# Kernel optimization log

Hardware: AMD Instinct MI355X
Metric: run time of the kernel (lower is better)

## Reference

```python
import jax, jax.numpy as jnp
import numpy as np

N = 50000      # nodes
E = 800000     # edges (avg degree 16)
IN = 64        # in_channels
OUT = 64       # out_channels
K = 3          # Chebyshev order
LAM = 2.0      # lambda_max for sym normalization


def setup_inputs() -> dict:
    key = jax.random.key(0)
    ks = jax.random.split(key, 16)
    s_in = 1.0 / np.sqrt(IN)
    s_out = 1.0 / np.sqrt(OUT)
    inp = {
        "X": jax.random.normal(ks[0], (N, IN), jnp.float32),
        "edge_index": jax.random.randint(ks[1], (2, E), 0, N, dtype=jnp.int64),
        "edge_weight": jax.random.uniform(ks[2], (E,), jnp.float32),
        # six ChebConv weight stacks [K, in, out] and biases [out]
        "W_xz": jax.random.normal(ks[3], (K, IN, OUT), jnp.float32) * s_in,
        "W_hz": jax.random.normal(ks[4], (K, OUT, OUT), jnp.float32) * s_out,
        "W_xr": jax.random.normal(ks[5], (K, IN, OUT), jnp.float32) * s_in,
        "W_hr": jax.random.normal(ks[6], (K, OUT, OUT), jnp.float32) * s_out,
        "W_xh": jax.random.normal(ks[7], (K, IN, OUT), jnp.float32) * s_in,
        "W_hh": jax.random.normal(ks[8], (K, OUT, OUT), jnp.float32) * s_out,
        "b_xz": jnp.zeros((OUT,), jnp.float32),
        "b_hz": jnp.zeros((OUT,), jnp.float32),
        "b_xr": jnp.zeros((OUT,), jnp.float32),
        "b_hr": jnp.zeros((OUT,), jnp.float32),
        "b_xh": jnp.zeros((OUT,), jnp.float32),
        "b_hh": jnp.zeros((OUT,), jnp.float32),
    }
    return inp


def _cheb_norm(edge_index, edge_weight):
    # PyG ChebConv __norm__ with sym normalization, lambda_max = 2:
    # L_hat = (2/lam) * (I - D^-1/2 A D^-1/2) - I
    src, dst = edge_index[0], edge_index[1]
    deg = jax.ops.segment_sum(edge_weight, src, num_segments=N)
    dinv = jnp.where(deg > 0, jax.lax.rsqrt(jnp.where(deg > 0, deg, 1.0)), 0.0)
    w_off = -(2.0 / LAM) * edge_weight * dinv[src] * dinv[dst]
    diag = 2.0 / LAM - 1.0  # 0 when lambda_max == 2
    return src, dst, w_off, diag


def _spmm(x, src, dst, w_off, diag):
    # y[i] = sum_{e: dst[e]=i} w_off[e] * x[src[e]] + diag * x[i]
    msg = w_off[:, None] * x[src]
    return jax.ops.segment_sum(msg, dst, num_segments=N) + diag * x


def _cheb_conv(x, W, b, src, dst, w_off, diag):
    Tx0 = x
    out = Tx0 @ W[0]
    Tx1 = _spmm(Tx0, src, dst, w_off, diag)
    out = out + Tx1 @ W[1]
    for k in range(2, K):
        Tx2 = 2.0 * _spmm(Tx1, src, dst, w_off, diag) - Tx0
        out = out + Tx2 @ W[k]
        Tx0, Tx1 = Tx1, Tx2
    return out + b


def reference(X, edge_index, edge_weight,
              W_xz, W_hz, W_xr, W_hr, W_xh, W_hh,
              b_xz, b_hz, b_xr, b_hr, b_xh, b_hh):
    src, dst, w_off, diag = _cheb_norm(edge_index, edge_weight)
    cheb = lambda x, W, b: _cheb_conv(x, W, b, src, dst, w_off, diag)
    H = jnp.zeros((N, OUT), X.dtype)  # _set_hidden_state with H=None
    Z = jax.nn.sigmoid(cheb(X, W_xz, b_xz) + cheb(H, W_hz, b_hz))
    R = jax.nn.sigmoid(cheb(X, W_xr, b_xr) + cheb(H, W_hr, b_hr))
    H_tilde = jnp.tanh(cheb(X, W_xh, b_xh) + cheb(H * R, W_hh, b_hh))
    H_new = Z * H + (1.0 - Z) * H_tilde
    return H_new
```

## Files before the change

### kernel.cpp

```cpp
#include <hip/hip_runtime.h>


#define N_NODES 50000
#define E_EDGES 800000
#define NC 64
#define BSH 6
#define BUKN 64
#define NBUK 782
#define EPB 2048
#define NBLK 391

#define OFF_CV       0
#define OFF_ROWSTART 1600000
#define OFF_TOTD     1650016
#define OFF_BASED    1650800
#define OFF_TOTS     1651584
#define OFF_BASES    1652368
#define OFF_TX1      1653152
#define OFF_RECD     1653152
#define OFF_DINV     3253152
#define OFF_CNTD     3303168
#define OFF_TX2      4853152
#define OFF_RECS     4853152
#define OFF_CNTS     6453152
#define OFF_WB       8053152

typedef __attribute__((ext_vector_type(8))) short bf16x8;
typedef __attribute__((ext_vector_type(4))) float f32x4;

__device__ __forceinline__ unsigned bf16rne(float x) {
    unsigned u = __float_as_uint(x);
    return (u + 0x7fffu + ((u >> 16) & 1u)) >> 16;
}

__global__ __launch_bounds__(256) void k_hist(const int* __restrict__ ei,
        int* __restrict__ cntD, int* __restrict__ cntS) {
    __shared__ int hD[NBUK], hS[NBUK];
    int t = threadIdx.x, blk = blockIdx.x;
    for (int b = t; b < NBUK; b += 256) { hD[b] = 0; hS[b] = 0; }
    __syncthreads();
    int e0 = blk * EPB;
    #pragma unroll
    for (int i = 0; i < 8; ++i) {
        int e = e0 + i * 256 + t;
        if (e < E_EDGES) {
            atomicAdd(&hS[ei[e] >> BSH], 1);
            atomicAdd(&hD[ei[E_EDGES + e] >> BSH], 1);
        }
    }
    __syncthreads();
    for (int b = t; b < NBUK; b += 256) {
        cntD[b * NBLK + blk] = hD[b];
        cntS[b * NBLK + blk] = hS[b];
    }
}

__global__ __launch_bounds__(256) void k_scanPB(int* __restrict__ cntD,
        int* __restrict__ cntS, int* __restrict__ totD, int* __restrict__ totS) {
    __shared__ int s[512];
    int t = threadIdx.x;
    int row = blockIdx.x; int* cnt; int* tot;
    if (row < NBUK) { cnt = cntD; tot = totD; }
    else            { row -= NBUK; cnt = cntS; tot = totS; }
    int v0 = (t < NBLK) ? cnt[row * NBLK + t] : 0;
    int v1 = (256 + t < NBLK) ? cnt[row * NBLK + 256 + t] : 0;
    s[t] = v0; s[256 + t] = v1;
    __syncthreads();
    for (int off = 1; off < 512; off <<= 1) {
        int a = (t >= off) ? s[t - off] : 0;
        int b = (256 + t >= off) ? s[256 + t - off] : 0;
        __syncthreads();
        s[t] += a; s[256 + t] += b;
        __syncthreads();
    }
    if (t < NBLK) cnt[row * NBLK + t] = s[t] - v0;
    if (256 + t < NBLK) cnt[row * NBLK + 256 + t] = s[256 + t] - v1;
    if (t == 0) tot[row] = s[511];
}

__global__ __launch_bounds__(256) void k_scanTot(int* __restrict__ totD,
        int* __restrict__ baseD, int* __restrict__ totS, int* __restrict__ baseS) {
    __shared__ int s[1024];
    int t = threadIdx.x;
    int* tot  = blockIdx.x ? totS  : totD;
    int* base = blockIdx.x ? baseS : baseD;
    int v[4];
    #pragma unroll
    for (int q = 0; q < 4; ++q) {
        int i = q * 256 + t;
        v[q] = (i < NBUK) ? tot[i] : 0;
        s[i] = v[q];
    }
    __syncthreads();
    for (int off = 1; off < 1024; off <<= 1) {
        int a[4];
        #pragma unroll
        for (int q = 0; q < 4; ++q) {
            int i = q * 256 + t;
            a[q] = (i >= off) ? s[i - off] : 0;
        }
        __syncthreads();
        #pragma unroll
        for (int q = 0; q < 4; ++q) s[q * 256 + t] += a[q];
        __syncthreads();
    }
    #pragma unroll
    for (int q = 0; q < 4; ++q) {
        int i = q * 256 + t;
        if (i < NBUK) base[i] = s[i] - v[q];
    }
}

__global__ __launch_bounds__(256) void k_scatter(const int* __restrict__ ei,
        const float* __restrict__ ew, const int* __restrict__ offD,
        const int* __restrict__ offS, const int* __restrict__ baseD,
        const int* __restrict__ baseS, long long* __restrict__ recD,
        long long* __restrict__ recS) {
    __shared__ int curD[NBUK], curS[NBUK];
    int t = threadIdx.x, blk = blockIdx.x;
    for (int b = t; b < NBUK; b += 256) {
        curD[b] = baseD[b] + offD[b * NBLK + blk];
        curS[b] = baseS[b] + offS[b * NBLK + blk];
    }
    __syncthreads();
    int e0 = blk * EPB;
    #pragma unroll
    for (int i = 0; i < 8; ++i) {
        int e = e0 + i * 256 + t;
        if (e < E_EDGES) {
            int sN = ei[e], dN = ei[E_EDGES + e];
            long long wb = (long long)(unsigned)__float_as_uint(ew[e]) << 32;
            int pD = atomicAdd(&curD[dN >> BSH], 1);
            recD[pD] = wb | (unsigned)((sN << BSH) | (dN & (BUKN - 1)));
            int pS = atomicAdd(&curS[sN >> BSH], 1);
            recS[pS] = wb | (unsigned)(sN & (BUKN - 1));
        }
    }
}

__global__ __launch_bounds__(256) void k_deg(const long long* __restrict__ recS,
        const int* __restrict__ totS, const int* __restrict__ baseS,
        float* __restrict__ dinv) {
    __shared__ float degL[BUKN];
    int t = threadIdx.x, b = blockIdx.x;
    if (t < BUKN) degL[t] = 0.f;
    __syncthreads();
    int st = baseS[b], n = totS[b];
    for (int i = t; i < n; i += 256) {
        long long r = recS[st + i];
        atomicAdd(&degL[(int)(r & (BUKN - 1))], __uint_as_float((unsigned)(r >> 32)));
    }
    __syncthreads();
    if (t < BUKN) {
        int node = b * BUKN + t;
        if (node < N_NODES) {
            float dg = degL[t];
            dinv[node] = dg > 0.f ? rsqrtf(dg) : 0.f;
        }
    }
}

__global__ __launch_bounds__(256) void k_csr(const long long* __restrict__ recD,
        const int* __restrict__ totD, const int* __restrict__ baseD,
        const float* __restrict__ dinv, long long* __restrict__ cv,
        int* __restrict__ row_start) {
    __shared__ int cnt[BUKN], rb[BUKN], cur[BUKN];
    __shared__ float dL[BUKN];
    int t = threadIdx.x, b = blockIdx.x;
    if (t < BUKN) {
        cnt[t] = 0;
        int node = b * BUKN + t;
        dL[t] = (node < N_NODES) ? dinv[node] : 0.f;
    }
    __syncthreads();
    int st = baseD[b], n = totD[b];
    for (int i = t; i < n; i += 256)
        atomicAdd(&cnt[(int)(recD[st + i] & (BUKN - 1))], 1);
    __syncthreads();
    if (t < BUKN) {
        int x = cnt[t];
        int orig = x;
        #pragma unroll
        for (int off = 1; off < BUKN; off <<= 1) {
            int v = __shfl_up(x, off, 64);
            if ((t & 63) >= off) x += v;
        }
        rb[t] = x - orig;
        cur[t] = x - orig;
        int node = b * BUKN + t;
        if (node < N_NODES) row_start[node] = st + (x - orig);
    }
    if (b == 0 && t == 0) row_start[N_NODES] = E_EDGES;
    __syncthreads();
    for (int i = t; i < n; i += 256) {
        long long r = recD[st + i];
        int m = (int)(r & 0xffffffffLL);
        float w = __uint_as_float((unsigned)(r >> 32));
        int rr = m & (BUKN - 1);
        int sN = m >> BSH;
        float val = -w * dinv[sN] * dL[rr];
        int pos = st + atomicAdd(&cur[rr], 1);
        cv[pos] = ((long long)__float_as_int(val) << 32) | (unsigned)sN;
    }
}

template<int SCALE, int SUB>
__global__ __launch_bounds__(256) void k_spmm(
        const int* __restrict__ row_start, const long long* __restrict__ cv,
        const float* __restrict__ xin, const float* __restrict__ xprev,
        float* __restrict__ out) {
    int wid = (blockIdx.x << 2) + (threadIdx.x >> 6);
    int lane = threadIdx.x & 63;
    if (wid >= N_NODES) return;
    int start = row_start[wid];
    int end   = row_start[wid + 1];
    float acc = 0.f;
    #pragma unroll 4
    for (int j = start; j < end; ++j) {
        long long p = cv[j];
        int s = (int)(p & 0xffffffffLL);
        float wv = __int_as_float((int)(p >> 32));
        acc = fmaf(wv, xin[(size_t)s * NC + lane], acc);
    }
    float r = (float)SCALE * acc;
    if (SUB) r -= xprev[(size_t)wid * NC + lane];
    out[(size_t)wid * NC + lane] = r;
}

__global__ __launch_bounds__(256) void k_prepw(const float* __restrict__ Wz,
        const float* __restrict__ Wh, short* __restrict__ WB) {
    int mg = blockIdx.x;
    int m = mg >> 1, g = mg & 1;
    const float* W = (g ? Wh : Wz) + m * 4096;
    int t = threadIdx.x;
    #pragma unroll
    for (int r = 0; r < 16; ++r) {
        int idx = r * 256 + t;
        int c = idx >> 6, o = idx & 63;
        float x = W[idx];
        unsigned hi = bf16rne(x);
        float fhi = __uint_as_float(hi << 16);
        unsigned lo = bf16rne(x - fhi);
        WB[(mg * 2 + 0) * 4096 + o * 64 + c] = (short)hi;
        WB[(mg * 2 + 1) * 4096 + o * 64 + c] = (short)lo;
    }
}

__global__ __launch_bounds__(256) void k_gru(
        const float* __restrict__ X, const float* __restrict__ Tx1,
        const float* __restrict__ Tx2, const short* __restrict__ WB,
        const float* __restrict__ bxz, const float* __restrict__ bhz,
        const float* __restrict__ bxh, const float* __restrict__ bhh,
        float* __restrict__ out) {
    __shared__ short Ahi[64 * 64];
    __shared__ short Alo[64 * 64];
    int tid = threadIdx.x;
    int l = tid & 63;
    int w = tid >> 6;
    int node0 = blockIdx.x * 64;

    f32x4 accz[4], acch[4];
    #pragma unroll
    for (int mt = 0; mt < 4; ++mt) {
        accz[mt] = (f32x4){0.f, 0.f, 0.f, 0.f};
        acch[mt] = (f32x4){0.f, 0.f, 0.f, 0.f};
    }

    const float* ins[3] = {X, Tx1, Tx2};
    #pragma unroll 1
    for (int m = 0; m < 3; ++m) {
        __syncthreads();
        const float* ip = ins[m];
        #pragma unroll
        for (int r = 0; r < 4; ++r) {
            int fidx = r * 256 + tid;
            int n = fidx >> 4, c4 = fidx & 15;
            int gn = node0 + n;
            float4 v = make_float4(0.f, 0.f, 0.f, 0.f);
            if (gn < N_NODES) v = *(const float4*)&ip[(size_t)gn * 64 + c4 * 4];
            unsigned h0 = bf16rne(v.x), h1 = bf16rne(v.y),
                     h2 = bf16rne(v.z), h3 = bf16rne(v.w);
            unsigned q0 = bf16rne(v.x - __uint_as_float(h0 << 16));
            unsigned q1 = bf16rne(v.y - __uint_as_float(h1 << 16));
            unsigned q2 = bf16rne(v.z - __uint_as_float(h2 << 16));
            unsigned q3 = bf16rne(v.w - __uint_as_float(h3 << 16));
            int kk = (c4 * 4) ^ ((n & 7) << 3);
            *(uint2*)&Ahi[n * 64 + kk] = make_uint2(h0 | (h1 << 16), h2 | (h3 << 16));
            *(uint2*)&Alo[n * 64 + kk] = make_uint2(q0 | (q1 << 16), q2 | (q3 << 16));
        }
        __syncthreads();
        const short* wbm = WB + m * 4 * 4096;
        #pragma unroll
        for (int kt = 0; kt < 2; ++kt) {
            int k0 = kt * 32 + (l >> 4) * 8;
            bf16x8 ah[4], al[4];
            #pragma unroll
            for (int mt = 0; mt < 4; ++mt) {
                int row = mt * 16 + (l & 15);
                int kk = k0 ^ ((row & 7) << 3);
                ah[mt] = *(const bf16x8*)&Ahi[row * 64 + kk];
                al[mt] = *(const bf16x8*)&Alo[row * 64 + kk];
            }
            int o = w * 16 + (l & 15);
            {
                bf16x8 bh_ = *(const bf16x8*)&wbm[0 * 4096 + o * 64 + k0];
                bf16x8 bl_ = *(const bf16x8*)&wbm[1 * 4096 + o * 64 + k0];
                #pragma unroll
                for (int mt = 0; mt < 4; ++mt) {
                    accz[mt] = __builtin_amdgcn_mfma_f32_16x16x32_bf16(ah[mt], bh_, accz[mt], 0, 0, 0);
                    accz[mt] = __builtin_amdgcn_mfma_f32_16x16x32_bf16(ah[mt], bl_, accz[mt], 0, 0, 0);
                    accz[mt] = __builtin_amdgcn_mfma_f32_16x16x32_bf16(al[mt], bh_, accz[mt], 0, 0, 0);
                }
            }
            {
                bf16x8 bh_ = *(const bf16x8*)&wbm[2 * 4096 + o * 64 + k0];
                bf16x8 bl_ = *(const bf16x8*)&wbm[3 * 4096 + o * 64 + k0];
                #pragma unroll
                for (int mt = 0; mt < 4; ++mt) {
                    acch[mt] = __builtin_amdgcn_mfma_f32_16x16x32_bf16(ah[mt], bh_, acch[mt], 0, 0, 0);
                    acch[mt] = __builtin_amdgcn_mfma_f32_16x16x32_bf16(ah[mt], bl_, acch[mt], 0, 0, 0);
                    acch[mt] = __builtin_amdgcn_mfma_f32_16x16x32_bf16(al[mt], bh_, acch[mt], 0, 0, 0);
                }
            }
        }
    }

    int o = w * 16 + (l & 15);
    float bz = bxz[o] + bhz[o];
    float bh = bxh[o] + bhh[o];
    #pragma unroll
    for (int mt = 0; mt < 4; ++mt) {
        #pragma unroll
        for (int r = 0; r < 4; ++r) {
            int node = node0 + mt * 16 + (l >> 4) * 4 + r;
            if (node < N_NODES) {
                float z = accz[mt][r] + bz;
                float h = acch[mt][r] + bh;
                float sig = 1.f / (1.f + __expf(-z));
                float e2 = __expf(-2.f * h);
                float th = (1.f - e2) / (1.f + e2);
                out[(size_t)node * 64 + o] = (1.f - sig) * th;
            }
        }
    }
}

extern "C" void kernel_launch(void* const* d_in, const int* in_sizes, int n_in,
                              void* d_out, int out_size, void* d_ws, size_t ws_size,
                              hipStream_t stream) {
    const float* X   = (const float*)d_in[0];
    const int*   ei  = (const int*)d_in[1];
    const float* ew  = (const float*)d_in[2];
    const float* Wxz = (const float*)d_in[3];
    const float* Wxh = (const float*)d_in[7];
    const float* bxz = (const float*)d_in[9];
    const float* bhz = (const float*)d_in[10];
    const float* bxh = (const float*)d_in[13];
    const float* bhh = (const float*)d_in[14];
    float* out = (float*)d_out;

    float* ws_f = (float*)d_ws;
    int*   ws_i = (int*)d_ws;

    long long* cv       = (long long*)(ws_i + OFF_CV);
    int*       rowstart = ws_i + OFF_ROWSTART;
    int*       totD     = ws_i + OFF_TOTD;
    int*       baseD    = ws_i + OFF_BASED;
    int*       totS     = ws_i + OFF_TOTS;
    int*       baseS    = ws_i + OFF_BASES;
    float*     tx1      = ws_f + OFF_TX1;
    long long* recD     = (long long*)(ws_i + OFF_RECD);
    float*     dinv     = ws_f + OFF_DINV;
    int*       cntD     = ws_i + OFF_CNTD;
    float*     tx2      = ws_f + OFF_TX2;
    long long* recS     = (long long*)(ws_i + OFF_RECS);
    int*       cntS     = ws_i + OFF_CNTS;
    short*     WB       = (short*)(ws_i + OFF_WB);

    const int TB = 256;
    k_prepw<<<6, TB, 0, stream>>>(Wxz, Wxh, WB);
    k_hist<<<NBLK, TB, 0, stream>>>(ei, cntD, cntS);
    k_scanPB<<<2 * NBUK, TB, 0, stream>>>(cntD, cntS, totD, totS);
    k_scanTot<<<2, TB, 0, stream>>>(totD, baseD, totS, baseS);
    k_scatter<<<NBLK, TB, 0, stream>>>(ei, ew, cntD, cntS, baseD, baseS, recD, recS);
    k_deg<<<NBUK, TB, 0, stream>>>(recS, totS, baseS, dinv);
    k_csr<<<NBUK, TB, 0, stream>>>(recD, totD, baseD, dinv, cv, rowstart);

    k_spmm<1, 0><<<(N_NODES + 3) / 4, TB, 0, stream>>>(rowstart, cv, X, X, tx1);
    k_spmm<2, 1><<<(N_NODES + 3) / 4, TB, 0, stream>>>(rowstart, cv, tx1, X, tx2);

    k_gru<<<NBUK, TB, 0, stream>>>(X, tx1, tx2, WB, bxz, bhz, bxh, bhh, out);
}
```

Measured before the change: 165.2 us.

## Store adjacency in padded ELL format with CSR overflow and fuse weight prep

The CSR build now writes the first 48 neighbours of each node into a fixed-width ELL array, zero-padded, and sends any further edges to the CSR array as overflow. The SpMM kernel runs a fully unrolled 48-slot loop that issues eight gathers at once for memory-level parallelism, then processes the overflow from CSR. Weight bf16 splitting is folded into extra blocks of the histogram kernel, which removes one launch. With an average degree of 16, the ELL array is mostly padding, so each SpMM pass reads about three times more index data and does many gathers of row 0 for the padded slots.

```diff
diff --git a/kernel.cpp b/kernel.cpp
--- a/kernel.cpp
+++ b/kernel.cpp
@@ -9,6 +9,7 @@
 #define NBUK 782
 #define EPB 2048
 #define NBLK 391
+#define ELLW 48
 
 #define OFF_CV       0
 #define OFF_ROWSTART 1600000
@@ -24,6 +25,7 @@
 #define OFF_RECS     4853152
 #define OFF_CNTS     6453152
 #define OFF_WB       8053152
+#define OFF_ELL      8077824
 
 typedef __attribute__((ext_vector_type(8))) short bf16x8;
 typedef __attribute__((ext_vector_type(4))) float f32x4;
@@ -34,9 +36,28 @@
 }
 
 __global__ __launch_bounds__(256) void k_hist(const int* __restrict__ ei,
-        int* __restrict__ cntD, int* __restrict__ cntS) {
+        int* __restrict__ cntD, int* __restrict__ cntS,
+        const float* __restrict__ Wz, const float* __restrict__ Wh,
+        short* __restrict__ WB) {
+    int t = threadIdx.x, blk = blockIdx.x;
+    if (blk >= NBLK) {
+        int mg = blk - NBLK;
+        int m = mg >> 1, g = mg & 1;
+        const float* W = (g ? Wh : Wz) + m * 4096;
+        #pragma unroll
+        for (int r = 0; r < 16; ++r) {
+            int idx = r * 256 + t;
+            int c = idx >> 6, o = idx & 63;
+            float x = W[idx];
+            unsigned hi = bf16rne(x);
+            float fhi = __uint_as_float(hi << 16);
+            unsigned lo = bf16rne(x - fhi);
+            WB[(mg * 2 + 0) * 4096 + o * 64 + c] = (short)hi;
+            WB[(mg * 2 + 1) * 4096 + o * 64 + c] = (short)lo;
+        }
+        return;
+    }
     __shared__ int hD[NBUK], hS[NBUK];
-    int t = threadIdx.x, blk = blockIdx.x;
     for (int b = t; b < NBUK; b += 256) { hD[b] = 0; hS[b] = 0; }
     __syncthreads();
     int e0 = blk * EPB;
@@ -163,12 +184,13 @@
 __global__ __launch_bounds__(256) void k_csr(const long long* __restrict__ recD,
         const int* __restrict__ totD, const int* __restrict__ baseD,
         const float* __restrict__ dinv, long long* __restrict__ cv,
-        int* __restrict__ row_start) {
+        long long* __restrict__ ell, int* __restrict__ row_start) {
     __shared__ int cnt[BUKN], rb[BUKN], cur[BUKN];
     __shared__ float dL[BUKN];
     int t = threadIdx.x, b = blockIdx.x;
     if (t < BUKN) {
         cnt[t] = 0;
+        cur[t] = 0;
         int node = b * BUKN + t;
         dL[t] = (node < N_NODES) ? dinv[node] : 0.f;
     }
@@ -186,7 +208,6 @@
             if ((t & 63) >= off) x += v;
         }
         rb[t] = x - orig;
-        cur[t] = x - orig;
         int node = b * BUKN + t;
         if (node < N_NODES) row_start[node] = st + (x - orig);
     }
@@ -199,51 +220,53 @@
         int rr = m & (BUKN - 1);
         int sN = m >> BSH;
         float val = -w * dinv[sN] * dL[rr];
-        int pos = st + atomicAdd(&cur[rr], 1);
-        cv[pos] = ((long long)__float_as_int(val) << 32) | (unsigned)sN;
+        long long rec = ((long long)__float_as_int(val) << 32) | (unsigned)sN;
+        int k = atomicAdd(&cur[rr], 1);
+        if (k < ELLW) ell[(size_t)(b * BUKN + rr) * ELLW + k] = rec;
+        else          cv[st + rb[rr] + k] = rec;
+    }
+    __syncthreads();
+    for (int idx = t; idx < BUKN * ELLW; idx += 256) {
+        int rr = idx / ELLW, k = idx - rr * ELLW;
+        if (k >= cnt[rr]) ell[(size_t)(b * BUKN + rr) * ELLW + k] = 0LL;
     }
 }
 
 template<int SCALE, int SUB>
 __global__ __launch_bounds__(256) void k_spmm(
-        const int* __restrict__ row_start, const long long* __restrict__ cv,
-        const float* __restrict__ xin, const float* __restrict__ xprev,
-        float* __restrict__ out) {
+        const int* __restrict__ row_start, const long long* __restrict__ ell,
+        const long long* __restrict__ cv, const float* __restrict__ xin,
+        const float* __restrict__ xprev, float* __restrict__ out) {
     int wid = (blockIdx.x << 2) + (threadIdx.x >> 6);
     int lane = threadIdx.x & 63;
     if (wid >= N_NODES) return;
+    const long long* er = ell + (size_t)wid * ELLW;
+    float acc = 0.f;
+    #pragma unroll
+    for (int c = 0; c < ELLW; c += 8) {
+        long long p[8];
+        #pragma unroll
+        for (int k = 0; k < 8; ++k) p[k] = er[c + k];
+        float xv[8];
+        #pragma unroll
+        for (int k = 0; k < 8; ++k)
+            xv[k] = xin[(size_t)(unsigned)(p[k] & 0xffffffffLL) * NC + lane];
+        #pragma unroll
+        for (int k = 0; k < 8; ++k)
+            acc = fmaf(__int_as_float((int)(p[k] >> 32)), xv[k], acc);
+    }
     int start = row_start[wid];
     int end   = row_start[wid + 1];
-    float acc = 0.f;
-    #pragma unroll 4
-    for (int j = start; j < end; ++j) {
-        long long p = cv[j];
-        int s = (int)(p & 0xffffffffLL);
-        float wv = __int_as_float((int)(p >> 32));
-        acc = fmaf(wv, xin[(size_t)s * NC + lane], acc);
+    if (end - start > ELLW) {
+        for (int j = start + ELLW; j < end; ++j) {
+            long long p = cv[j];
+            int s = (int)(p & 0xffffffffLL);
+            acc = fmaf(__int_as_float((int)(p >> 32)), xin[(size_t)s * NC + lane], acc);
+        }
     }
     float r = (float)SCALE * acc;
     if (SUB) r -= xprev[(size_t)wid * NC + lane];
     out[(size_t)wid * NC + lane] = r;
-}
-
-__global__ __launch_bounds__(256) void k_prepw(const float* __restrict__ Wz,
-        const float* __restrict__ Wh, short* __restrict__ WB) {
-    int mg = blockIdx.x;
-    int m = mg >> 1, g = mg & 1;
-    const float* W = (g ? Wh : Wz) + m * 4096;
-    int t = threadIdx.x;
-    #pragma unroll
-    for (int r = 0; r < 16; ++r) {
-        int idx = r * 256 + t;
-        int c = idx >> 6, o = idx & 63;
-        float x = W[idx];
-        unsigned hi = bf16rne(x);
-        float fhi = __uint_as_float(hi << 16);
-        unsigned lo = bf16rne(x - fhi);
-        WB[(mg * 2 + 0) * 4096 + o * 64 + c] = (short)hi;
-        WB[(mg * 2 + 1) * 4096 + o * 64 + c] = (short)lo;
-    }
 }
 
 __global__ __launch_bounds__(256) void k_gru(
@@ -376,18 +399,18 @@
     long long* recS     = (long long*)(ws_i + OFF_RECS);
     int*       cntS     = ws_i + OFF_CNTS;
     short*     WB       = (short*)(ws_i + OFF_WB);
+    long long* ell      = (long long*)(ws_i + OFF_ELL);
 
     const int TB = 256;
-    k_prepw<<<6, TB, 0, stream>>>(Wxz, Wxh, WB);
-    k_hist<<<NBLK, TB, 0, stream>>>(ei, cntD, cntS);
+    k_hist<<<NBLK + 6, TB, 0, stream>>>(ei, cntD, cntS, Wxz, Wxh, WB);
     k_scanPB<<<2 * NBUK, TB, 0, stream>>>(cntD, cntS, totD, totS);
     k_scanTot<<<2, TB, 0, stream>>>(totD, baseD, totS, baseS);
     k_scatter<<<NBLK, TB, 0, stream>>>(ei, ew, cntD, cntS, baseD, baseS, recD, recS);
     k_deg<<<NBUK, TB, 0, stream>>>(recS, totS, baseS, dinv);
-    k_csr<<<NBUK, TB, 0, stream>>>(recD, totD, baseD, dinv, cv, rowstart);
-
-    k_spmm<1, 0><<<(N_NODES + 3) / 4, TB, 0, stream>>>(rowstart, cv, X, X, tx1);
-    k_spmm<2, 1><<<(N_NODES + 3) / 4, TB, 0, stream>>>(rowstart, cv, tx1, X, tx2);
+    k_csr<<<NBUK, TB, 0, stream>>>(recD, totD, baseD, dinv, cv, ell, rowstart);
+
+    k_spmm<1, 0><<<(N_NODES + 3) / 4, TB, 0, stream>>>(rowstart, ell, cv, X, X, tx1);
+    k_spmm<2, 1><<<(N_NODES + 3) / 4, TB, 0, stream>>>(rowstart, ell, cv, tx1, X, tx2);
 
     k_gru<<<NBUK, TB, 0, stream>>>(X, tx1, tx2, WB, bxz, bhz, bxh, bhh, out);
 }
```

Result: slower. 197.4 us (+19.5%).

## Vectorize SpMM gathers with float4 edge-parallel lanes and fold weight prep into hist

Applied to the files above, without the earlier changes.

The SpMM kernel now splits each wavefront into four sub-groups of 16 lanes. Each sub-group handles a different edge and gathers a float4 slice of the source row, two edges per iteration, and the partial sums are combined with xor shuffles. This raises memory-level parallelism and gather width compared with one scalar load per lane per edge. Separately, the weight bf16 split kernel is merged into the histogram launch as extra blocks, which removes one kernel launch. An unused shared array is also dropped.

```diff
diff --git a/kernel.cpp b/kernel.cpp
--- a/kernel.cpp
+++ b/kernel.cpp
@@ -34,9 +34,28 @@
 }
 
 __global__ __launch_bounds__(256) void k_hist(const int* __restrict__ ei,
-        int* __restrict__ cntD, int* __restrict__ cntS) {
+        int* __restrict__ cntD, int* __restrict__ cntS,
+        const float* __restrict__ Wz, const float* __restrict__ Wh,
+        short* __restrict__ WB) {
+    int t = threadIdx.x, blk = blockIdx.x;
+    if (blk >= NBLK) {
+        int mg = blk - NBLK;
+        int m = mg >> 1, g = mg & 1;
+        const float* W = (g ? Wh : Wz) + m * 4096;
+        #pragma unroll
+        for (int r = 0; r < 16; ++r) {
+            int idx = r * 256 + t;
+            int c = idx >> 6, o = idx & 63;
+            float x = W[idx];
+            unsigned hi = bf16rne(x);
+            float fhi = __uint_as_float(hi << 16);
+            unsigned lo = bf16rne(x - fhi);
+            WB[(mg * 2 + 0) * 4096 + o * 64 + c] = (short)hi;
+            WB[(mg * 2 + 1) * 4096 + o * 64 + c] = (short)lo;
+        }
+        return;
+    }
     __shared__ int hD[NBUK], hS[NBUK];
-    int t = threadIdx.x, blk = blockIdx.x;
     for (int b = t; b < NBUK; b += 256) { hD[b] = 0; hS[b] = 0; }
     __syncthreads();
     int e0 = blk * EPB;
@@ -164,7 +183,7 @@
         const int* __restrict__ totD, const int* __restrict__ baseD,
         const float* __restrict__ dinv, long long* __restrict__ cv,
         int* __restrict__ row_start) {
-    __shared__ int cnt[BUKN], rb[BUKN], cur[BUKN];
+    __shared__ int cnt[BUKN], cur[BUKN];
     __shared__ float dL[BUKN];
     int t = threadIdx.x, b = blockIdx.x;
     if (t < BUKN) {
@@ -185,7 +204,6 @@
             int v = __shfl_up(x, off, 64);
             if ((t & 63) >= off) x += v;
         }
-        rb[t] = x - orig;
         cur[t] = x - orig;
         int node = b * BUKN + t;
         if (node < N_NODES) row_start[node] = st + (x - orig);
@@ -210,39 +228,49 @@
         const float* __restrict__ xin, const float* __restrict__ xprev,
         float* __restrict__ out) {
     int wid = (blockIdx.x << 2) + (threadIdx.x >> 6);
-    int lane = threadIdx.x & 63;
+    int l = threadIdx.x & 63;
     if (wid >= N_NODES) return;
     int start = row_start[wid];
     int end   = row_start[wid + 1];
-    float acc = 0.f;
-    #pragma unroll 4
-    for (int j = start; j < end; ++j) {
-        long long p = cv[j];
-        int s = (int)(p & 0xffffffffLL);
-        float wv = __int_as_float((int)(p >> 32));
-        acc = fmaf(wv, xin[(size_t)s * NC + lane], acc);
-    }
-    float r = (float)SCALE * acc;
-    if (SUB) r -= xprev[(size_t)wid * NC + lane];
-    out[(size_t)wid * NC + lane] = r;
-}
-
-__global__ __launch_bounds__(256) void k_prepw(const float* __restrict__ Wz,
-        const float* __restrict__ Wh, short* __restrict__ WB) {
-    int mg = blockIdx.x;
-    int m = mg >> 1, g = mg & 1;
-    const float* W = (g ? Wh : Wz) + m * 4096;
-    int t = threadIdx.x;
-    #pragma unroll
-    for (int r = 0; r < 16; ++r) {
-        int idx = r * 256 + t;
-        int c = idx >> 6, o = idx & 63;
-        float x = W[idx];
-        unsigned hi = bf16rne(x);
-        float fhi = __uint_as_float(hi << 16);
-        unsigned lo = bf16rne(x - fhi);
-        WB[(mg * 2 + 0) * 4096 + o * 64 + c] = (short)hi;
-        WB[(mg * 2 + 1) * 4096 + o * 64 + c] = (short)lo;
+    int sub = l >> 4;
+    int q   = l & 15;
+    float4 acc = make_float4(0.f, 0.f, 0.f, 0.f);
+    for (int j = start; j < end; j += 8) {
+        int jA = j + sub;
+        int jB = j + 4 + sub;
+        long long pA = (jA < end) ? cv[jA] : 0LL;
+        long long pB = (jB < end) ? cv[jB] : 0LL;
+        float4 xA = *(const float4*)&xin[(size_t)(unsigned)(pA & 0xffffffffLL) * NC + q * 4];
+        float4 xB = *(const float4*)&xin[(size_t)(unsigned)(pB & 0xffffffffLL) * NC + q * 4];
+        float vA = __int_as_float((int)(pA >> 32));
+        float vB = __int_as_float((int)(pB >> 32));
+        acc.x = fmaf(vA, xA.x, acc.x);
+        acc.y = fmaf(vA, xA.y, acc.y);
+        acc.z = fmaf(vA, xA.z, acc.z);
+        acc.w = fmaf(vA, xA.w, acc.w);
+        acc.x = fmaf(vB, xB.x, acc.x);
+        acc.y = fmaf(vB, xB.y, acc.y);
+        acc.z = fmaf(vB, xB.z, acc.z);
+        acc.w = fmaf(vB, xB.w, acc.w);
+    }
+    #pragma unroll
+    for (int m = 16; m <= 32; m <<= 1) {
+        acc.x += __shfl_xor(acc.x, m, 64);
+        acc.y += __shfl_xor(acc.y, m, 64);
+        acc.z += __shfl_xor(acc.z, m, 64);
+        acc.w += __shfl_xor(acc.w, m, 64);
+    }
+    if (sub == 0) {
+        float4 r;
+        r.x = (float)SCALE * acc.x;
+        r.y = (float)SCALE * acc.y;
+        r.z = (float)SCALE * acc.z;
+        r.w = (float)SCALE * acc.w;
+        if (SUB) {
+            float4 xo = *(const float4*)&xprev[(size_t)wid * NC + q * 4];
+            r.x -= xo.x; r.y -= xo.y; r.z -= xo.z; r.w -= xo.w;
+        }
+        *(float4*)&out[(size_t)wid * NC + q * 4] = r;
     }
 }
 
@@ -378,8 +406,7 @@
     short*     WB       = (short*)(ws_i + OFF_WB);
 
     const int TB = 256;
-    k_prepw<<<6, TB, 0, stream>>>(Wxz, Wxh, WB);
-    k_hist<<<NBLK, TB, 0, stream>>>(ei, cntD, cntS);
+    k_hist<<<NBLK + 6, TB, 0, stream>>>(ei, cntD, cntS, Wxz, Wxh, WB);
     k_scanPB<<<2 * NBUK, TB, 0, stream>>>(cntD, cntS, totD, totS);
     k_scanTot<<<2, TB, 0, stream>>>(totD, baseD, totS, baseS);
     k_scatter<<<NBLK, TB, 0, stream>>>(ei, ew, cntD, cntS, baseD, baseS, recD, recS);
```

New measurement: 147.1 us, median of 2. -11.0%, faster.
